# Performance work log

Hardware: AMD Instinct MI355X
Metric: run time of the kernel (lower is better)

## Reference

```python
import jax, jax.numpy as jnp
import numpy as np

D_MODEL = 1024
EXPERT_DIM = 2048
N_EXPERTS = 8
LN_EPS = 1e-5


def _bit_quant(W):
    # W: [out, in] (or [..., out, in]); per-output-row ternary quantization with STE
    scale = jnp.clip(jnp.mean(jnp.abs(W), axis=-1, keepdims=True), 1e-5, None)
    w_q = jnp.clip(jnp.round(W / scale), -1.0, 1.0) * scale
    return W + jax.lax.stop_gradient(w_q - W)


def setup_inputs() -> dict:
    key = jax.random.key(0)
    ks = jax.random.split(key, 7)
    x = jax.random.normal(ks[0], (4, 2048, D_MODEL), dtype=jnp.float32)
    # kaiming_normal fan_out, linear -> std = 1/sqrt(out_features)
    shared_w1 = jax.random.normal(ks[1], (EXPERT_DIM, D_MODEL), dtype=jnp.float32) / np.sqrt(EXPERT_DIM)
    shared_w2 = jax.random.normal(ks[2], (D_MODEL, EXPERT_DIM), dtype=jnp.float32) / np.sqrt(D_MODEL)
    expert_w1 = jax.random.normal(ks[3], (N_EXPERTS, EXPERT_DIM, D_MODEL), dtype=jnp.float32) / np.sqrt(EXPERT_DIM)
    expert_w2 = jax.random.normal(ks[4], (N_EXPERTS, D_MODEL, EXPERT_DIM), dtype=jnp.float32) / np.sqrt(D_MODEL)
    router_w = 0.02 * jax.random.normal(ks[5], (N_EXPERTS, D_MODEL), dtype=jnp.float32)
    ln_gamma = jnp.ones((D_MODEL,), dtype=jnp.float32)
    ln_beta = jnp.zeros((D_MODEL,), dtype=jnp.float32)
    return {"x": x, "shared_w1": shared_w1, "shared_w2": shared_w2,
            "expert_w1": expert_w1, "expert_w2": expert_w2,
            "router_w": router_w, "ln_gamma": ln_gamma, "ln_beta": ln_beta}


def reference(x, shared_w1, shared_w2, expert_w1, expert_w2, router_w, ln_gamma, ln_beta):
    # LayerNorm
    mu = jnp.mean(x, axis=-1, keepdims=True)
    var = jnp.mean(jnp.square(x - mu), axis=-1, keepdims=True)
    h = (x - mu) / jnp.sqrt(var + LN_EPS) * ln_gamma + ln_beta  # [B,T,D]

    # Shared expert (BitLinear -> SiLU -> BitLinear)
    sw1, sw2 = _bit_quant(shared_w1), _bit_quant(shared_w2)
    shared_out = jax.nn.silu(jnp.einsum('btd,fd->btf', h, sw1)) @ sw2.T  # [B,T,D]

    # Top-1 router
    probs = jax.nn.softmax(h @ router_w.T, axis=-1)  # [B,T,E]
    top_prob = jnp.max(probs, axis=-1)               # [B,T]
    top_idx = jnp.argmax(probs, axis=-1)             # [B,T]

    # Routed experts: compute all experts densely, select via one-hot gate
    ew1, ew2 = _bit_quant(expert_w1), _bit_quant(expert_w2)
    h1 = jax.nn.silu(jnp.einsum('btd,efd->ebtf', h, ew1))      # [E,B,T,F]
    eo = jnp.einsum('ebtf,edf->ebtd', h1, ew2)                 # [E,B,T,D]
    gate = jax.nn.one_hot(top_idx, N_EXPERTS, dtype=h.dtype) * top_prob[..., None]  # [B,T,E]
    routed_out = jnp.einsum('ebtd,bte->btd', eo, gate)

    return shared_out + routed_out
```

## Files before the change

### kernel.cpp

```cpp
#include <hip/hip_runtime.h>
#include <hip/hip_bf16.h>

#define D_MODEL 1024
#define F_DIM   2048
#define NE      8
#define NTOK    8192
#define MAXT    72
#define HBLK    32

typedef __attribute__((ext_vector_type(8))) short bf16x8;
typedef __attribute__((ext_vector_type(4))) float f32x4;

__device__ __forceinline__ unsigned short f2b(float f) {
    unsigned int u = __float_as_uint(f);
    u += 0x7FFFu + ((u >> 16) & 1u);
    return (unsigned short)(u >> 16);
}
__device__ __forceinline__ unsigned int pack2(float a, float b) {
    return (unsigned int)f2b(a) | ((unsigned int)f2b(b) << 16);
}
__device__ __forceinline__ void async16(const void* g, void* l) {
    __builtin_amdgcn_global_load_lds((const __attribute__((address_space(1))) void*)g,
                                     (__attribute__((address_space(3))) void*)l, 16, 0, 0);
}

template <int K>
__device__ __forceinline__ void quant_wave(const float* __restrict__ W,
                                           unsigned short* __restrict__ Q,
                                           int row) {
    constexpr int PV = K / 256;
    const int lane = threadIdx.x & 63;
    const float4* Wv = (const float4*)(W + (size_t)row * K);
    float4 v[PV];
#pragma unroll
    for (int i = 0; i < PV; i++) v[i] = Wv[lane + 64 * i];
    float s = 0.f;
#pragma unroll
    for (int i = 0; i < PV; i++)
        s += fabsf(v[i].x) + fabsf(v[i].y) + fabsf(v[i].z) + fabsf(v[i].w);
#pragma unroll
    for (int o = 32; o > 0; o >>= 1) s += __shfl_down(s, o);
    s = __shfl(s, 0);
    const float scale = fmaxf(s * (1.0f / K), 1e-5f);
    const float inv = 1.0f / scale;
    unsigned int* Qu = (unsigned int*)(Q + (size_t)row * K);
#pragma unroll
    for (int i = 0; i < PV; i++) {
        float q0 = fminf(1.f, fmaxf(-1.f, rintf(v[i].x * inv))) * scale;
        float q1 = fminf(1.f, fmaxf(-1.f, rintf(v[i].y * inv))) * scale;
        float q2 = fminf(1.f, fmaxf(-1.f, rintf(v[i].z * inv))) * scale;
        float q3 = fminf(1.f, fmaxf(-1.f, rintf(v[i].w * inv))) * scale;
        Qu[2 * (lane + 64 * i)]     = pack2(q0, q1);
        Qu[2 * (lane + 64 * i) + 1] = pack2(q2, q3);
    }
}

__device__ __forceinline__ void ln_dev(const float* __restrict__ x,
                                       const float* __restrict__ gamma,
                                       const float* __restrict__ beta,
                                       const float* __restrict__ rw,
                                       unsigned short* __restrict__ h,
                                       int* __restrict__ top_idx,
                                       float* __restrict__ top_prob,
                                       int blk) {
    const int lane = threadIdx.x & 63;
    const size_t tok = (size_t)blk * 4 + (threadIdx.x >> 6);

    const float4* xr = (const float4*)(x + tok * D_MODEL);
    float4 xv[4];
#pragma unroll
    for (int i = 0; i < 4; i++) xv[i] = xr[lane + 64 * i];
    float s = 0.f, q = 0.f;
#pragma unroll
    for (int i = 0; i < 4; i++) {
        s += xv[i].x + xv[i].y + xv[i].z + xv[i].w;
        q += xv[i].x * xv[i].x + xv[i].y * xv[i].y + xv[i].z * xv[i].z + xv[i].w * xv[i].w;
    }
#pragma unroll
    for (int o = 32; o > 0; o >>= 1) { s += __shfl_down(s, o); q += __shfl_down(q, o); }
    s = __shfl(s, 0); q = __shfl(q, 0);
    const float mean = s * (1.0f / D_MODEL);
    const float rstd = rsqrtf(q * (1.0f / D_MODEL) - mean * mean + 1e-5f);

    float4 hv[4];
    unsigned int* hr = (unsigned int*)(h + tok * D_MODEL);
#pragma unroll
    for (int i = 0; i < 4; i++) {
        const float4 g  = ((const float4*)gamma)[lane + 64 * i];
        const float4 bt = ((const float4*)beta)[lane + 64 * i];
        hv[i].x = (xv[i].x - mean) * rstd * g.x + bt.x;
        hv[i].y = (xv[i].y - mean) * rstd * g.y + bt.y;
        hv[i].z = (xv[i].z - mean) * rstd * g.z + bt.z;
        hv[i].w = (xv[i].w - mean) * rstd * g.w + bt.w;
        hr[2 * (lane + 64 * i)]     = pack2(hv[i].x, hv[i].y);
        hr[2 * (lane + 64 * i) + 1] = pack2(hv[i].z, hv[i].w);
    }

    float acc[NE];
#pragma unroll
    for (int e = 0; e < NE; e++) {
        const float4* rr = (const float4*)(rw + e * D_MODEL);
        float a = 0.f;
#pragma unroll
        for (int i = 0; i < 4; i++) {
            const float4 r = rr[lane + 64 * i];
            a += hv[i].x * r.x + hv[i].y * r.y + hv[i].z * r.z + hv[i].w * r.w;
        }
        acc[e] = a;
    }
#pragma unroll
    for (int e = 0; e < NE; e++) {
#pragma unroll
        for (int o = 32; o > 0; o >>= 1) acc[e] += __shfl_down(acc[e], o);
    }
    if (lane == 0) {
        float m = acc[0]; int bi = 0;
#pragma unroll
        for (int e = 1; e < NE; e++) { if (acc[e] > m) { m = acc[e]; bi = e; } }
        float se = 0.f;
#pragma unroll
        for (int e = 0; e < NE; e++) se += __expf(acc[e] - m);
        top_idx[tok]  = bi;
        top_prob[tok] = 1.0f / se;
    }
}

__global__ __launch_bounds__(256) void fused_pre(const float* __restrict__ sw1,
                                                 const float* __restrict__ sw2,
                                                 const float* __restrict__ ew1,
                                                 const float* __restrict__ ew2,
                                                 unsigned short* __restrict__ sw1q,
                                                 unsigned short* __restrict__ sw2q,
                                                 unsigned short* __restrict__ ew1q,
                                                 unsigned short* __restrict__ ew2q,
                                                 const float* __restrict__ x,
                                                 const float* __restrict__ gamma,
                                                 const float* __restrict__ beta,
                                                 const float* __restrict__ rw,
                                                 unsigned short* __restrict__ h,
                                                 int* __restrict__ top_idx,
                                                 float* __restrict__ top_prob) {
    const int b = blockIdx.x;
    const int w = threadIdx.x >> 6;
    if (b < 512)        quant_wave<1024>(sw1, sw1q, b * 4 + w);
    else if (b < 768)   quant_wave<2048>(sw2, sw2q, (b - 512) * 4 + w);
    else if (b < 4864)  quant_wave<1024>(ew1, ew1q, (b - 768) * 4 + w);
    else if (b < 6912)  quant_wave<2048>(ew2, ew2q, (b - 4864) * 4 + w);
    else                ln_dev(x, gamma, beta, rw, h, top_idx, top_prob, b - 6912);
}

__global__ __launch_bounds__(256) void hist_kernel(const int* __restrict__ top_idx,
                                                   int* __restrict__ blockhist) {
    __shared__ int lh[NE];
    if (threadIdx.x < NE) lh[threadIdx.x] = 0;
    __syncthreads();
    const int t = blockIdx.x * 256 + threadIdx.x;
    atomicAdd(&lh[top_idx[t]], 1);
    __syncthreads();
    if (threadIdx.x < NE) blockhist[blockIdx.x * NE + threadIdx.x] = lh[threadIdx.x];
}

__global__ __launch_bounds__(256) void scan_plan(const int* __restrict__ blockhist,
                                                 int* __restrict__ base,
                                                 int4* __restrict__ tilemap,
                                                 int* __restrict__ tok_perm) {
    __shared__ int sh[HBLK * NE];
    __shared__ int counts[NE];
    __shared__ int offsets[NE];
    __shared__ int tstart[NE + 1];
    const int tid = threadIdx.x;
    sh[tid] = blockhist[tid];
    __syncthreads();
    if (tid < NE) {
        int c = 0;
#pragma unroll
        for (int b = 0; b < HBLK; b++) c += sh[b * NE + tid];
        counts[tid] = c;
    }
    __syncthreads();
    if (tid == 0) {
        int off = 0, slot = 0;
#pragma unroll
        for (int e = 0; e < NE; e++) {
            offsets[e] = off;
            tstart[e] = slot;
            slot += (counts[e] + 127) >> 7;
            off += counts[e];
        }
        tstart[NE] = slot;
    }
    __syncthreads();
    if (tid < MAXT) {
        int4 t; t.x = 0; t.y = 0; t.z = 0; t.w = 0;
#pragma unroll
        for (int e = 0; e < NE; e++) {
            if (tid >= tstart[e] && tid < tstart[e + 1]) {
                const int k = (tid - tstart[e]) << 7;
                t.x = e; t.y = offsets[e] + k; t.z = min(128, counts[e] - k);
            }
        }
        tilemap[tid] = t;
    }
    {
        const int b = tid >> 3, e = tid & 7;
        int r = offsets[e];
        for (int bb = 0; bb < b; bb++) r += sh[bb * NE + e];
        base[b * NE + e] = r;
    }
    if (tid < 128) tok_perm[NTOK + tid] = 0;
}

__global__ __launch_bounds__(256) void scatter_tokens(const int* __restrict__ top_idx,
                                                      const float* __restrict__ top_prob,
                                                      const int* __restrict__ base,
                                                      int* __restrict__ tok_perm,
                                                      float* __restrict__ probg) {
    __shared__ int cur[NE];
    if (threadIdx.x < NE) cur[threadIdx.x] = base[blockIdx.x * NE + threadIdx.x];
    __syncthreads();
    const int t = blockIdx.x * 256 + threadIdx.x;
    const int e = top_idx[t];
    const int pos = atomicAdd(&cur[e], 1);
    tok_perm[pos] = t;
    probg[pos] = top_prob[t];
}

template <int MODE>
__global__ __launch_bounds__(256) void gemm64(const unsigned short* __restrict__ A,
                                              const unsigned short* __restrict__ Bmain,
                                              const unsigned short* __restrict__ Bexp,
                                              unsigned short* __restrict__ C1s,
                                              unsigned short* __restrict__ C1r,
                                              float* __restrict__ Out,
                                              int N, int K,
                                              const int4* __restrict__ tilemap,
                                              const int* __restrict__ tok_perm,
                                              const float* __restrict__ probg) {
    constexpr unsigned GX = (MODE == 0) ? (F_DIM / 128) : (D_MODEL / 128);
    const unsigned flat = blockIdx.y * GX + blockIdx.x;
    const unsigned nwg  = gridDim.y * GX;
    const unsigned swz  = (flat & 7u) * (nwg >> 3) + (flat >> 3);
    const unsigned bx   = swz & (GX - 1u);
    const unsigned by   = swz / GX;

    int m0, rowsValid;
    const unsigned short* B;
    unsigned short* Cb = nullptr;
    bool gather = false;
    if (MODE == 0) {
        if (by < 64) {
            m0 = by * 128; rowsValid = 128; B = Bmain; Cb = C1s;
        } else {
            int4 tm = tilemap[by - 64];
            if (tm.z == 0) return;
            m0 = tm.y; rowsValid = tm.z;
            B = Bexp + (size_t)tm.x * F_DIM * D_MODEL;
            Cb = C1r; gather = true;
        }
    } else if (MODE == 1) {
        int4 tm = tilemap[by];
        if (tm.z == 0) return;
        m0 = tm.y; rowsValid = tm.z;
        B = Bmain + (size_t)tm.x * D_MODEL * F_DIM;
    } else {
        m0 = by * 128; rowsValid = 128; B = Bmain;
    }
    const int n0 = bx * 128;

    __shared__ unsigned short As[128 * 64];
    __shared__ unsigned short Bs[128 * 64];

    const int tid = threadIdx.x;
    const int lane = tid & 63;
    const int w = tid >> 6;
    const int wm = w >> 1, wn = w & 1;

    f32x4 acc[4][4];
#pragma unroll
    for (int i = 0; i < 4; i++)
#pragma unroll
        for (int j = 0; j < 4; j++) acc[i][j] = (f32x4){0.f, 0.f, 0.f, 0.f};

    const int sRow = lane >> 3;
    const int sCol = ((lane & 7) ^ sRow) * 8;
    const unsigned short* aP[4];
    const unsigned short* bP[4];
#pragma unroll
    for (int qq = 0; qq < 4; qq++) {
        const int ra = w * 32 + qq * 8 + sRow;
        size_t arow;
        if (MODE == 0) arow = gather ? (size_t)tok_perm[m0 + ra] : (size_t)(m0 + ra);
        else           arow = (size_t)(m0 + ra);
        aP[qq] = A + arow * (size_t)K + sCol;
        bP[qq] = B + (size_t)(n0 + ra) * K + sCol;
    }
    unsigned short* aL = As + w * 2048;
    unsigned short* bL = Bs + w * 2048;

    const int fr = lane & 15, fq = lane >> 4;
    const bf16x8* Ar = (const bf16x8*)As;
    const bf16x8* Br = (const bf16x8*)Bs;

    for (int k0 = 0; k0 < K; k0 += 64) {
#pragma unroll
        for (int qq = 0; qq < 4; qq++) async16(aP[qq] + k0, aL + qq * 512);
#pragma unroll
        for (int qq = 0; qq < 4; qq++) async16(bP[qq] + k0, bL + qq * 512);
        __syncthreads();
#pragma unroll
        for (int kc = 0; kc < 2; kc++) {
            bf16x8 af[4], bfr[4];
#pragma unroll
            for (int i = 0; i < 4; i++) {
                const int row = wm * 64 + i * 16 + fr;
                af[i] = Ar[row * 8 + (((kc << 2) + fq) ^ (fr & 7))];
            }
#pragma unroll
            for (int j = 0; j < 4; j++) {
                const int row = wn * 64 + j * 16 + fr;
                bfr[j] = Br[row * 8 + (((kc << 2) + fq) ^ (fr & 7))];
            }
#pragma unroll
            for (int i = 0; i < 4; i++)
#pragma unroll
                for (int j = 0; j < 4; j++)
                    acc[i][j] = __builtin_amdgcn_mfma_f32_16x16x32_bf16(af[i], bfr[j], acc[i][j], 0, 0, 0);
        }
        __syncthreads();
    }

#pragma unroll
    for (int i = 0; i < 4; i++) {
        const int rb = wm * 64 + i * 16 + fq * 4;
#pragma unroll
        for (int t = 0; t < 4; t++) {
            const int r = rb + t;
            if (r < rowsValid) {
#pragma unroll
                for (int j = 0; j < 4; j++) {
                    const int c = n0 + wn * 64 + j * 16 + fr;
                    float v = acc[i][j][t];
                    if (MODE == 0) {
                        const float den = 1.0f + __expf(-v);
                        v = v * __builtin_amdgcn_rcpf(den);
                        Cb[(size_t)(m0 + r) * N + c] = f2b(v);
                    } else if (MODE == 1) {
                        const int tokr = tok_perm[m0 + r];
                        Out[(size_t)tokr * N + c] = probg[m0 + r] * v;
                    } else {
                        float* o = Out + (size_t)(m0 + r) * N + c;
                        *o = *o + v;
                    }
                }
            }
        }
    }
}

extern "C" void kernel_launch(void* const* d_in, const int* in_sizes, int n_in,
                              void* d_out, int out_size, void* d_ws, size_t ws_size,
                              hipStream_t stream) {
    const float* x   = (const float*)d_in[0];
    const float* sw1 = (const float*)d_in[1];
    const float* sw2 = (const float*)d_in[2];
    const float* ew1 = (const float*)d_in[3];
    const float* ew2 = (const float*)d_in[4];
    const float* rw  = (const float*)d_in[5];
    const float* gam = (const float*)d_in[6];
    const float* bet = (const float*)d_in[7];
    float* out = (float*)d_out;

    char* ws = (char*)d_ws;
    const size_t H_OFF    = 0;
    const size_t SW1Q_OFF = H_OFF + (size_t)NTOK * D_MODEL * 2;
    const size_t SW2Q_OFF = SW1Q_OFF + (size_t)F_DIM * D_MODEL * 2;
    const size_t EW1Q_OFF = SW2Q_OFF + (size_t)D_MODEL * F_DIM * 2;
    const size_t EW2Q_OFF = EW1Q_OFF + (size_t)NE * F_DIM * D_MODEL * 2;
    const size_t H1S_OFF  = EW2Q_OFF + (size_t)NE * D_MODEL * F_DIM * 2;
    const size_t H1R_OFF  = H1S_OFF + (size_t)NTOK * F_DIM * 2;
    const size_t PERM_OFF = H1R_OFF + (size_t)(NTOK + 128) * F_DIM * 2;
    const size_t PROBG_OFF = PERM_OFF + (NTOK + 128) * 4;
    const size_t IDX_OFF   = PROBG_OFF + (NTOK + 128) * 4;
    const size_t PROB_OFF  = IDX_OFF + NTOK * 4;
    const size_t BH_OFF    = PROB_OFF + NTOK * 4;
    const size_t BASE_OFF  = BH_OFF + HBLK * NE * 4;
    const size_t TILE_OFF  = BASE_OFF + HBLK * NE * 4;

    unsigned short* h     = (unsigned short*)(ws + H_OFF);
    unsigned short* sw1q  = (unsigned short*)(ws + SW1Q_OFF);
    unsigned short* sw2q  = (unsigned short*)(ws + SW2Q_OFF);
    unsigned short* ew1q  = (unsigned short*)(ws + EW1Q_OFF);
    unsigned short* ew2q  = (unsigned short*)(ws + EW2Q_OFF);
    unsigned short* h1s   = (unsigned short*)(ws + H1S_OFF);
    unsigned short* h1r   = (unsigned short*)(ws + H1R_OFF);
    int*   tok_perm = (int*)(ws + PERM_OFF);
    float* probg    = (float*)(ws + PROBG_OFF);
    int*   idx      = (int*)(ws + IDX_OFF);
    float* prob     = (float*)(ws + PROB_OFF);
    int*   blockhist = (int*)(ws + BH_OFF);
    int*   base      = (int*)(ws + BASE_OFF);
    int4*  tilemap   = (int4*)(ws + TILE_OFF);

    fused_pre<<<8960, 256, 0, stream>>>(sw1, sw2, ew1, ew2, sw1q, sw2q, ew1q, ew2q,
                                        x, gam, bet, rw, h, idx, prob);

    hist_kernel<<<HBLK, 256, 0, stream>>>(idx, blockhist);
    scan_plan<<<1, 256, 0, stream>>>(blockhist, base, tilemap, tok_perm);
    scatter_tokens<<<HBLK, 256, 0, stream>>>(idx, prob, base, tok_perm, probg);

    gemm64<0><<<dim3(F_DIM / 128, 64 + MAXT), 256, 0, stream>>>(
        h, sw1q, ew1q, h1s, h1r, nullptr, F_DIM, D_MODEL, tilemap, tok_perm, nullptr);

    gemm64<1><<<dim3(D_MODEL / 128, MAXT), 256, 0, stream>>>(
        h1r, ew2q, nullptr, nullptr, nullptr, out, D_MODEL, F_DIM, tilemap, tok_perm, probg);
    gemm64<2><<<dim3(D_MODEL / 128, NTOK / 128), 256, 0, stream>>>(
        h1s, sw2q, nullptr, nullptr, nullptr, out, D_MODEL, F_DIM, tilemap, tok_perm, probg);
}
```

Baseline: 426.1 us.

## Split preprocessing kernels, merge routing plan into one block, widen quant stores

Splits the fused quantize+LayerNorm kernel into separate ln_router and quant_all launches. The three routing kernels (histogram, scan, scatter) become a single one-block plan_all kernel, which drops two launches and the global blockhist/base buffers. The quantizer now loads two adjacent float4s per lane and writes one 16-byte bf16 store instead of two 4-byte stores. The cost is a serial single-workgroup scatter loop with many barriers, and one more launch boundary on the quant/LN side.

Measured after the change: 442.1 us. 3.8% more time.

```diff
diff --git a/kernel.cpp b/kernel.cpp
--- a/kernel.cpp
+++ b/kernel.cpp
@@ -28,43 +28,69 @@
 __device__ __forceinline__ void quant_wave(const float* __restrict__ W,
                                            unsigned short* __restrict__ Q,
                                            int row) {
-    constexpr int PV = K / 256;
+    constexpr int NP = K / 512;
     const int lane = threadIdx.x & 63;
     const float4* Wv = (const float4*)(W + (size_t)row * K);
-    float4 v[PV];
-#pragma unroll
-    for (int i = 0; i < PV; i++) v[i] = Wv[lane + 64 * i];
+    float4 a[NP], b[NP];
+#pragma unroll
+    for (int i = 0; i < NP; i++) {
+        a[i] = Wv[2 * (lane + 64 * i)];
+        b[i] = Wv[2 * (lane + 64 * i) + 1];
+    }
     float s = 0.f;
 #pragma unroll
-    for (int i = 0; i < PV; i++)
-        s += fabsf(v[i].x) + fabsf(v[i].y) + fabsf(v[i].z) + fabsf(v[i].w);
+    for (int i = 0; i < NP; i++) {
+        s += fabsf(a[i].x) + fabsf(a[i].y) + fabsf(a[i].z) + fabsf(a[i].w);
+        s += fabsf(b[i].x) + fabsf(b[i].y) + fabsf(b[i].z) + fabsf(b[i].w);
+    }
 #pragma unroll
     for (int o = 32; o > 0; o >>= 1) s += __shfl_down(s, o);
     s = __shfl(s, 0);
     const float scale = fmaxf(s * (1.0f / K), 1e-5f);
     const float inv = 1.0f / scale;
-    unsigned int* Qu = (unsigned int*)(Q + (size_t)row * K);
-#pragma unroll
-    for (int i = 0; i < PV; i++) {
-        float q0 = fminf(1.f, fmaxf(-1.f, rintf(v[i].x * inv))) * scale;
-        float q1 = fminf(1.f, fmaxf(-1.f, rintf(v[i].y * inv))) * scale;
-        float q2 = fminf(1.f, fmaxf(-1.f, rintf(v[i].z * inv))) * scale;
-        float q3 = fminf(1.f, fmaxf(-1.f, rintf(v[i].w * inv))) * scale;
-        Qu[2 * (lane + 64 * i)]     = pack2(q0, q1);
-        Qu[2 * (lane + 64 * i) + 1] = pack2(q2, q3);
-    }
-}
-
-__device__ __forceinline__ void ln_dev(const float* __restrict__ x,
-                                       const float* __restrict__ gamma,
-                                       const float* __restrict__ beta,
-                                       const float* __restrict__ rw,
-                                       unsigned short* __restrict__ h,
-                                       int* __restrict__ top_idx,
-                                       float* __restrict__ top_prob,
-                                       int blk) {
+    uint4* Qo = (uint4*)(Q + (size_t)row * K);
+#pragma unroll
+    for (int i = 0; i < NP; i++) {
+        float qa0 = fminf(1.f, fmaxf(-1.f, rintf(a[i].x * inv))) * scale;
+        float qa1 = fminf(1.f, fmaxf(-1.f, rintf(a[i].y * inv))) * scale;
+        float qa2 = fminf(1.f, fmaxf(-1.f, rintf(a[i].z * inv))) * scale;
+        float qa3 = fminf(1.f, fmaxf(-1.f, rintf(a[i].w * inv))) * scale;
+        float qb0 = fminf(1.f, fmaxf(-1.f, rintf(b[i].x * inv))) * scale;
+        float qb1 = fminf(1.f, fmaxf(-1.f, rintf(b[i].y * inv))) * scale;
+        float qb2 = fminf(1.f, fmaxf(-1.f, rintf(b[i].z * inv))) * scale;
+        float qb3 = fminf(1.f, fmaxf(-1.f, rintf(b[i].w * inv))) * scale;
+        uint4 o;
+        o.x = pack2(qa0, qa1); o.y = pack2(qa2, qa3);
+        o.z = pack2(qb0, qb1); o.w = pack2(qb2, qb3);
+        Qo[lane + 64 * i] = o;
+    }
+}
+
+__global__ __launch_bounds__(256) void quant_all(const float* __restrict__ sw1,
+                                                 const float* __restrict__ sw2,
+                                                 const float* __restrict__ ew1,
+                                                 const float* __restrict__ ew2,
+                                                 unsigned short* __restrict__ sw1q,
+                                                 unsigned short* __restrict__ sw2q,
+                                                 unsigned short* __restrict__ ew1q,
+                                                 unsigned short* __restrict__ ew2q) {
+    const int b = blockIdx.x;
+    const int w = threadIdx.x >> 6;
+    if (b < 512)        quant_wave<1024>(sw1, sw1q, b * 4 + w);
+    else if (b < 768)   quant_wave<2048>(sw2, sw2q, (b - 512) * 4 + w);
+    else if (b < 4864)  quant_wave<1024>(ew1, ew1q, (b - 768) * 4 + w);
+    else                quant_wave<2048>(ew2, ew2q, (b - 4864) * 4 + w);
+}
+
+__global__ __launch_bounds__(256) void ln_router(const float* __restrict__ x,
+                                                 const float* __restrict__ gamma,
+                                                 const float* __restrict__ beta,
+                                                 const float* __restrict__ rw,
+                                                 unsigned short* __restrict__ h,
+                                                 int* __restrict__ top_idx,
+                                                 float* __restrict__ top_prob) {
     const int lane = threadIdx.x & 63;
-    const size_t tok = (size_t)blk * 4 + (threadIdx.x >> 6);
+    const size_t tok = (size_t)blockIdx.x * 4 + (threadIdx.x >> 6);
 
     const float4* xr = (const float4*)(x + tok * D_MODEL);
     float4 xv[4];
@@ -125,56 +151,34 @@
     }
 }
 
-__global__ __launch_bounds__(256) void fused_pre(const float* __restrict__ sw1,
-                                                 const float* __restrict__ sw2,
-                                                 const float* __restrict__ ew1,
-                                                 const float* __restrict__ ew2,
-                                                 unsigned short* __restrict__ sw1q,
-                                                 unsigned short* __restrict__ sw2q,
-                                                 unsigned short* __restrict__ ew1q,
-                                                 unsigned short* __restrict__ ew2q,
-                                                 const float* __restrict__ x,
-                                                 const float* __restrict__ gamma,
-                                                 const float* __restrict__ beta,
-                                                 const float* __restrict__ rw,
-                                                 unsigned short* __restrict__ h,
-                                                 int* __restrict__ top_idx,
-                                                 float* __restrict__ top_prob) {
-    const int b = blockIdx.x;
-    const int w = threadIdx.x >> 6;
-    if (b < 512)        quant_wave<1024>(sw1, sw1q, b * 4 + w);
-    else if (b < 768)   quant_wave<2048>(sw2, sw2q, (b - 512) * 4 + w);
-    else if (b < 4864)  quant_wave<1024>(ew1, ew1q, (b - 768) * 4 + w);
-    else if (b < 6912)  quant_wave<2048>(ew2, ew2q, (b - 4864) * 4 + w);
-    else                ln_dev(x, gamma, beta, rw, h, top_idx, top_prob, b - 6912);
-}
-
-__global__ __launch_bounds__(256) void hist_kernel(const int* __restrict__ top_idx,
-                                                   int* __restrict__ blockhist) {
-    __shared__ int lh[NE];
-    if (threadIdx.x < NE) lh[threadIdx.x] = 0;
-    __syncthreads();
-    const int t = blockIdx.x * 256 + threadIdx.x;
-    atomicAdd(&lh[top_idx[t]], 1);
-    __syncthreads();
-    if (threadIdx.x < NE) blockhist[blockIdx.x * NE + threadIdx.x] = lh[threadIdx.x];
-}
-
-__global__ __launch_bounds__(256) void scan_plan(const int* __restrict__ blockhist,
-                                                 int* __restrict__ base,
-                                                 int4* __restrict__ tilemap,
-                                                 int* __restrict__ tok_perm) {
-    __shared__ int sh[HBLK * NE];
+__global__ __launch_bounds__(256) void plan_all(const int* __restrict__ top_idx,
+                                                const float* __restrict__ top_prob,
+                                                int4* __restrict__ tilemap,
+                                                int* __restrict__ tok_perm,
+                                                float* __restrict__ probg) {
+    __shared__ int bh[HBLK * NE];
     __shared__ int counts[NE];
     __shared__ int offsets[NE];
     __shared__ int tstart[NE + 1];
+    __shared__ int base_s[HBLK * NE];
+    __shared__ int cur[NE];
     const int tid = threadIdx.x;
-    sh[tid] = blockhist[tid];
+
+    bh[tid] = 0;
+    if (tid < 128) tok_perm[NTOK + tid] = 0;
     __syncthreads();
+
+#pragma unroll
+    for (int c = 0; c < HBLK; c++) {
+        const int t = c * 256 + tid;
+        atomicAdd(&bh[c * NE + top_idx[t]], 1);
+    }
+    __syncthreads();
+
     if (tid < NE) {
         int c = 0;
 #pragma unroll
-        for (int b = 0; b < HBLK; b++) c += sh[b * NE + tid];
+        for (int b = 0; b < HBLK; b++) c += bh[b * NE + tid];
         counts[tid] = c;
     }
     __syncthreads();
@@ -204,25 +208,21 @@
     {
         const int b = tid >> 3, e = tid & 7;
         int r = offsets[e];
-        for (int bb = 0; bb < b; bb++) r += sh[bb * NE + e];
-        base[b * NE + e] = r;
-    }
-    if (tid < 128) tok_perm[NTOK + tid] = 0;
-}
-
-__global__ __launch_bounds__(256) void scatter_tokens(const int* __restrict__ top_idx,
-                                                      const float* __restrict__ top_prob,
-                                                      const int* __restrict__ base,
-                                                      int* __restrict__ tok_perm,
-                                                      float* __restrict__ probg) {
-    __shared__ int cur[NE];
-    if (threadIdx.x < NE) cur[threadIdx.x] = base[blockIdx.x * NE + threadIdx.x];
+        for (int bb = 0; bb < b; bb++) r += bh[bb * NE + e];
+        base_s[b * NE + e] = r;
+    }
     __syncthreads();
-    const int t = blockIdx.x * 256 + threadIdx.x;
-    const int e = top_idx[t];
-    const int pos = atomicAdd(&cur[e], 1);
-    tok_perm[pos] = t;
-    probg[pos] = top_prob[t];
+
+    for (int c = 0; c < HBLK; c++) {
+        if (tid < NE) cur[tid] = base_s[c * NE + tid];
+        __syncthreads();
+        const int t = c * 256 + tid;
+        const int e = top_idx[t];
+        const int pos = atomicAdd(&cur[e], 1);
+        tok_perm[pos] = t;
+        probg[pos] = top_prob[t];
+        __syncthreads();
+    }
 }
 
 template <int MODE>
@@ -382,9 +382,7 @@
     const size_t PROBG_OFF = PERM_OFF + (NTOK + 128) * 4;
     const size_t IDX_OFF   = PROBG_OFF + (NTOK + 128) * 4;
     const size_t PROB_OFF  = IDX_OFF + NTOK * 4;
-    const size_t BH_OFF    = PROB_OFF + NTOK * 4;
-    const size_t BASE_OFF  = BH_OFF + HBLK * NE * 4;
-    const size_t TILE_OFF  = BASE_OFF + HBLK * NE * 4;
+    const size_t TILE_OFF  = PROB_OFF + NTOK * 4;
 
     unsigned short* h     = (unsigned short*)(ws + H_OFF);
     unsigned short* sw1q  = (unsigned short*)(ws + SW1Q_OFF);
@@ -397,16 +395,13 @@
     float* probg    = (float*)(ws + PROBG_OFF);
     int*   idx      = (int*)(ws + IDX_OFF);
     float* prob     = (float*)(ws + PROB_OFF);
-    int*   blockhist = (int*)(ws + BH_OFF);
-    int*   base      = (int*)(ws + BASE_OFF);
-    int4*  tilemap   = (int4*)(ws + TILE_OFF);
-
-    fused_pre<<<8960, 256, 0, stream>>>(sw1, sw2, ew1, ew2, sw1q, sw2q, ew1q, ew2q,
-                                        x, gam, bet, rw, h, idx, prob);
-
-    hist_kernel<<<HBLK, 256, 0, stream>>>(idx, blockhist);
-    scan_plan<<<1, 256, 0, stream>>>(blockhist, base, tilemap, tok_perm);
-    scatter_tokens<<<HBLK, 256, 0, stream>>>(idx, prob, base, tok_perm, probg);
+    int4*  tilemap  = (int4*)(ws + TILE_OFF);
+
+    ln_router<<<NTOK / 4, 256, 0, stream>>>(x, gam, bet, rw, h, idx, prob);
+
+    quant_all<<<6912, 256, 0, stream>>>(sw1, sw2, ew1, ew2, sw1q, sw2q, ew1q, ew2q);
+
+    plan_all<<<1, 256, 0, stream>>>(idx, prob, tilemap, tok_perm, probg);
 
     gemm64<0><<<dim3(F_DIM / 128, 64 + MAXT), 256, 0, stream>>>(
         h, sw1q, ew1q, h1s, h1r, nullptr, F_DIM, D_MODEL, tilemap, tok_perm, nullptr);
```

## Merge shared and routed down-projection GEMMs into one launch with atomic accumulation

Applied to the files above, without the earlier changes.

The shared-expert and routed-expert second GEMMs now run as a single launch covering 64+MAXT row tiles, with outputs accumulated into a zeroed output buffer via unsafeAtomicAdd. N and K become compile-time constants. This removes one kernel launch and the tail and serialization between the two down GEMMs, so both sets of tiles can fill the GPU together. The cost is a memset of the 32 MB output and float atomics on every output element, whose summation order is nondeterministic.

Result: slower. 527.2 us (+23.7%).

```diff
diff --git a/kernel.cpp b/kernel.cpp
--- a/kernel.cpp
+++ b/kernel.cpp
@@ -227,16 +227,18 @@
 
 template <int MODE>
 __global__ __launch_bounds__(256) void gemm64(const unsigned short* __restrict__ A,
+                                              const unsigned short* __restrict__ A2,
                                               const unsigned short* __restrict__ Bmain,
                                               const unsigned short* __restrict__ Bexp,
                                               unsigned short* __restrict__ C1s,
                                               unsigned short* __restrict__ C1r,
                                               float* __restrict__ Out,
-                                              int N, int K,
                                               const int4* __restrict__ tilemap,
                                               const int* __restrict__ tok_perm,
                                               const float* __restrict__ probg) {
-    constexpr unsigned GX = (MODE == 0) ? (F_DIM / 128) : (D_MODEL / 128);
+    constexpr int N = (MODE == 0) ? F_DIM : D_MODEL;
+    constexpr int K = (MODE == 0) ? D_MODEL : F_DIM;
+    constexpr unsigned GX = N / 128;
     const unsigned flat = blockIdx.y * GX + blockIdx.x;
     const unsigned nwg  = gridDim.y * GX;
     const unsigned swz  = (flat & 7u) * (nwg >> 3) + (flat >> 3);
@@ -245,25 +247,20 @@
 
     int m0, rowsValid;
     const unsigned short* B;
+    const unsigned short* Asrc = A;
     unsigned short* Cb = nullptr;
-    bool gather = false;
-    if (MODE == 0) {
-        if (by < 64) {
-            m0 = by * 128; rowsValid = 128; B = Bmain; Cb = C1s;
-        } else {
-            int4 tm = tilemap[by - 64];
-            if (tm.z == 0) return;
-            m0 = tm.y; rowsValid = tm.z;
-            B = Bexp + (size_t)tm.x * F_DIM * D_MODEL;
-            Cb = C1r; gather = true;
-        }
-    } else if (MODE == 1) {
-        int4 tm = tilemap[by];
+    bool routed = false;
+    if (by < 64) {
+        m0 = by * 128; rowsValid = 128; B = Bmain;
+        if (MODE == 0) Cb = C1s;
+    } else {
+        int4 tm = tilemap[by - 64];
         if (tm.z == 0) return;
         m0 = tm.y; rowsValid = tm.z;
-        B = Bmain + (size_t)tm.x * D_MODEL * F_DIM;
-    } else {
-        m0 = by * 128; rowsValid = 128; B = Bmain;
+        B = Bexp + (size_t)tm.x * F_DIM * D_MODEL;
+        routed = true;
+        if (MODE == 0) Cb = C1r;
+        else           Asrc = A2;
     }
     const int n0 = bx * 128;
 
@@ -289,9 +286,9 @@
     for (int qq = 0; qq < 4; qq++) {
         const int ra = w * 32 + qq * 8 + sRow;
         size_t arow;
-        if (MODE == 0) arow = gather ? (size_t)tok_perm[m0 + ra] : (size_t)(m0 + ra);
+        if (MODE == 0) arow = routed ? (size_t)tok_perm[m0 + ra] : (size_t)(m0 + ra);
         else           arow = (size_t)(m0 + ra);
-        aP[qq] = A + arow * (size_t)K + sCol;
+        aP[qq] = Asrc + arow * (size_t)K + sCol;
         bP[qq] = B + (size_t)(n0 + ra) * K + sCol;
     }
     unsigned short* aL = As + w * 2048;
@@ -344,12 +341,13 @@
                         const float den = 1.0f + __expf(-v);
                         v = v * __builtin_amdgcn_rcpf(den);
                         Cb[(size_t)(m0 + r) * N + c] = f2b(v);
-                    } else if (MODE == 1) {
-                        const int tokr = tok_perm[m0 + r];
-                        Out[(size_t)tokr * N + c] = probg[m0 + r] * v;
                     } else {
-                        float* o = Out + (size_t)(m0 + r) * N + c;
-                        *o = *o + v;
+                        if (routed) {
+                            const int tokr = tok_perm[m0 + r];
+                            unsafeAtomicAdd(Out + (size_t)tokr * N + c, probg[m0 + r] * v);
+                        } else {
+                            unsafeAtomicAdd(Out + (size_t)(m0 + r) * N + c, v);
+                        }
                     }
                 }
             }
@@ -401,6 +399,8 @@
     int*   base      = (int*)(ws + BASE_OFF);
     int4*  tilemap   = (int4*)(ws + TILE_OFF);
 
+    hipMemsetAsync(out, 0, (size_t)NTOK * D_MODEL * sizeof(float), stream);
+
     fused_pre<<<8960, 256, 0, stream>>>(sw1, sw2, ew1, ew2, sw1q, sw2q, ew1q, ew2q,
                                         x, gam, bet, rw, h, idx, prob);
 
@@ -409,10 +409,8 @@
     scatter_tokens<<<HBLK, 256, 0, stream>>>(idx, prob, base, tok_perm, probg);
 
     gemm64<0><<<dim3(F_DIM / 128, 64 + MAXT), 256, 0, stream>>>(
-        h, sw1q, ew1q, h1s, h1r, nullptr, F_DIM, D_MODEL, tilemap, tok_perm, nullptr);
-
-    gemm64<1><<<dim3(D_MODEL / 128, MAXT), 256, 0, stream>>>(
-        h1r, ew2q, nullptr, nullptr, nullptr, out, D_MODEL, F_DIM, tilemap, tok_perm, probg);
-    gemm64<2><<<dim3(D_MODEL / 128, NTOK / 128), 256, 0, stream>>>(
-        h1s, sw2q, nullptr, nullptr, nullptr, out, D_MODEL, F_DIM, tilemap, tok_perm, probg);
-}
+        h, nullptr, sw1q, ew1q, h1s, h1r, nullptr, tilemap, tok_perm, nullptr);
+
+    gemm64<1><<<dim3(D_MODEL / 128, 64 + MAXT), 256, 0, stream>>>(
+        h1s, h1r, sw2q, ew2q, nullptr, nullptr, out, tilemap, tok_perm, probg);
+}
```
